# Kernel optimization log

Measured on AMD Instinct MI355X. Metric: run time of the kernel, lower is better.

Reference implementation:

```python
import jax, jax.numpy as jnp
import numpy as np

INS, OUTS = 768, 64
B, S = 8, 2048


def setup_inputs() -> dict:
    key = jax.random.key(0)
    ks = jax.random.split(key, 7)
    scale = 1.0 / np.sqrt(INS)
    inputs = jax.random.normal(ks[0], (B, S, INS), dtype=jnp.float32)
    Wq = jax.random.uniform(ks[1], (INS, OUTS), jnp.float32, -scale, scale)
    bq = jax.random.uniform(ks[2], (OUTS,), jnp.float32, -scale, scale)
    Wk = jax.random.uniform(ks[3], (INS, OUTS), jnp.float32, -scale, scale)
    bk = jax.random.uniform(ks[4], (OUTS,), jnp.float32, -scale, scale)
    Wv = jax.random.uniform(ks[5], (INS, OUTS), jnp.float32, -scale, scale)
    bv = jax.random.uniform(ks[6], (OUTS,), jnp.float32, -scale, scale)
    return {"inputs": inputs, "Wq": Wq, "bq": bq, "Wk": Wk, "bk": bk, "Wv": Wv, "bv": bv}


def reference(inputs, Wq, bq, Wk, bk, Wv, bv):
    # QKV projections: [B, S, ins] @ [ins, outs] -> [B, S, outs]
    q = jnp.einsum('bsi,io->bso', inputs, Wq) + bq
    k = jnp.einsum('bsi,io->bso', inputs, Wk) + bk
    v = jnp.einsum('bsi,io->bso', inputs, Wv) + bv
    dim_k = k.shape[-1]
    # scores: [B, S, S] (materialized, as in the original bmm-based impl)
    att = jnp.einsum('bqd,bkd->bqk', q, k) / jnp.sqrt(jnp.asarray(dim_k, q.dtype))
    att_soft = jax.nn.softmax(att, axis=-1)
    out = jnp.einsum('bqk,bkd->bqd', att_soft, v)
    return out
```

## Files before the change

kernel.cpp:

```cpp
#include <hip/hip_runtime.h>
#include <hip/hip_bf16.h>
#include <stdint.h>

#define INS 768
#define OUTS 64
#define BB 8
#define SS 2048
#define LDP 40

typedef __attribute__((ext_vector_type(8))) short short8;
typedef __attribute__((ext_vector_type(4))) float f32x4;

__device__ inline unsigned short f2bf(float f) {
  union { float f; uint32_t u; } v; v.f = f;
  uint32_t r = v.u + 0x7FFFu + ((v.u >> 16) & 1u);
  return (unsigned short)(r >> 16);
}

__device__ inline short8 cvt8hw(float4 a, float4 b) {
  union { __hip_bfloat162 h[4]; short8 s; } u;
  u.h[0] = __float22bfloat162_rn(make_float2(a.x, a.y));
  u.h[1] = __float22bfloat162_rn(make_float2(a.z, a.w));
  u.h[2] = __float22bfloat162_rn(make_float2(b.x, b.y));
  u.h[3] = __float22bfloat162_rn(make_float2(b.z, b.w));
  return u.s;
}

__device__ inline void gl_lds16(const void* g, void* l) {
  __builtin_amdgcn_global_load_lds(
      (const __attribute__((address_space(1))) uint32_t*)g,
      (__attribute__((address_space(3))) uint32_t*)l, 16, 0, 0);
}

__device__ inline void memfence_sched() { asm volatile("" ::: "memory"); }

#define PIPE_BARRIER(N)                                        \
  do {                                                         \
    asm volatile("s_waitcnt vmcnt(" #N ")" ::: "memory");      \
    __builtin_amdgcn_s_barrier();                              \
    __builtin_amdgcn_sched_barrier(0);                         \
  } while (0)

__global__ __launch_bounds__(256) void prep(
    const float* __restrict__ Wq, const float* __restrict__ Wk,
    const float* __restrict__ Wv, unsigned short* __restrict__ WT) {
  const int idx = blockIdx.x * 256 + threadIdx.x;
  const int m = idx / (INS * OUTS);
  const int r = idx - m * (INS * OUTS);
  const int k = r >> 6, n = r & 63;
  const float* W = (m == 0) ? Wq : (m == 1) ? Wk : Wv;
  const float s = (m == 0) ? 0.125f : 1.0f;
  WT[((size_t)m * OUTS + n) * INS + k] = f2bf(W[(size_t)k * OUTS + n] * s);
}

__global__ __launch_bounds__(256) void qkv(
    const float* __restrict__ X, const unsigned short* __restrict__ WT,
    const float* __restrict__ bq, const float* __restrict__ bk,
    const float* __restrict__ bv,
    unsigned short* __restrict__ Qg, unsigned short* __restrict__ Kg,
    unsigned short* __restrict__ Vtg) {
  __shared__ __align__(16) float Xs[4][1024];
  const int tid  = threadIdx.x;
  const int wave = tid >> 6, lane = tid & 63;
  const int quad = lane >> 4, l16 = lane & 15;
  const int chg  = wave;
  const int row0 = blockIdx.x * 32;

  const int sr = tid >> 3, ss = tid & 7;
  const char* gsrc =
      (const char*)(X + (size_t)(row0 + sr) * INS) + ((ss ^ (sr & 7)) << 4);
  char* ldsb = (char*)&Xs[0][0] + wave * 1024;

  const float* Bm[3]; float scl[3]; int col0[3];
  const unsigned short* Wt[3];
#pragma unroll
  for (int nt = 0; nt < 3; ++nt) {
    const int n0 = chg * 48 + nt * 16;
    const int mat = n0 >> 6;
    col0[nt] = n0 & 63;
    Wt[nt] = WT + ((size_t)mat * OUTS + col0[nt] + l16) * INS + quad * 8;
    if (mat == 0)      { Bm[nt] = bq; scl[nt] = 0.125f; }
    else if (mat == 1) { Bm[nt] = bk; scl[nt] = 1.0f; }
    else               { Bm[nt] = bv; scl[nt] = 1.0f; }
  }

  int off0[2], off1[2];
#pragma unroll
  for (int fr = 0; fr < 2; ++fr) {
    const int lr = fr * 16 + l16;
    off0[fr] = lr * 128 + ((((quad << 1)    ) ^ (lr & 7)) << 4);
    off1[fr] = lr * 128 + ((((quad << 1) | 1) ^ (lr & 7)) << 4);
  }

  f32x4 acc[2][3];
#pragma unroll
  for (int fr = 0; fr < 2; ++fr)
#pragma unroll
    for (int nt = 0; nt < 3; ++nt) acc[fr][nt] = (f32x4){0.f, 0.f, 0.f, 0.f};

  short8 wb[3][3];

  gl_lds16(gsrc, ldsb);
#pragma unroll
  for (int nt = 0; nt < 3; ++nt)
    wb[0][nt] = *reinterpret_cast<const short8*>(Wt[nt]);
  memfence_sched();
  gl_lds16(gsrc + 128, ldsb + 4096);
  gl_lds16(gsrc + 256, ldsb + 8192);
#pragma unroll
  for (int nt = 0; nt < 3; ++nt)
    wb[1][nt] = *reinterpret_cast<const short8*>(Wt[nt] + 32);

#pragma unroll
  for (int kc = 0; kc < 24; ++kc) {
    if (kc <= 21)      PIPE_BARRIER(4);
    else if (kc == 22) PIPE_BARRIER(3);
    else               PIPE_BARRIER(0);

    const char* xb = (const char*)&Xs[0][0] + (kc & 3) * 4096;
    float4 f00 = *reinterpret_cast<const float4*>(xb + off0[0]);
    float4 f01 = *reinterpret_cast<const float4*>(xb + off1[0]);
    float4 f10 = *reinterpret_cast<const float4*>(xb + off0[1]);
    float4 f11 = *reinterpret_cast<const float4*>(xb + off1[1]);
    short8 a0 = cvt8hw(f00, f01);
    short8 a1 = cvt8hw(f10, f11);
#pragma unroll
    for (int nt = 0; nt < 3; ++nt) {
      acc[0][nt] = __builtin_amdgcn_mfma_f32_16x16x32_bf16(a0, wb[kc % 3][nt], acc[0][nt], 0, 0, 0);
      acc[1][nt] = __builtin_amdgcn_mfma_f32_16x16x32_bf16(a1, wb[kc % 3][nt], acc[1][nt], 0, 0, 0);
    }
    if (kc + 3 < 24)
      gl_lds16(gsrc + (size_t)(kc + 3) * 128, ldsb + (size_t)((kc + 3) & 3) * 4096);
    if (kc + 2 < 24) {
#pragma unroll
      for (int nt = 0; nt < 3; ++nt)
        wb[(kc + 2) % 3][nt] =
            *reinterpret_cast<const short8*>(Wt[nt] + (kc + 2) * 32);
    }
  }

#pragma unroll
  for (int fr = 0; fr < 2; ++fr) {
    const int gm0 = row0 + fr * 16 + quad * 4;
#pragma unroll
    for (int nt = 0; nt < 3; ++nt) {
      const int n = chg * 48 + nt * 16 + l16;
      const float bias = Bm[nt][col0[nt] + l16] * scl[nt];
      if (n < 128) {
        unsigned short* dstbase = (n < 64) ? Qg : Kg;
        const int nn = n & 63;
#pragma unroll
        for (int r = 0; r < 4; ++r)
          dstbase[(size_t)(gm0 + r) * OUTS + nn] = f2bf(acc[fr][nt][r] + bias);
      } else {
        const int d = n - 128;
        const int batch = gm0 >> 11, s0 = gm0 & 2047;
        ushort4 pk;
        pk.x = f2bf(acc[fr][nt][0] + bias);
        pk.y = f2bf(acc[fr][nt][1] + bias);
        pk.z = f2bf(acc[fr][nt][2] + bias);
        pk.w = f2bf(acc[fr][nt][3] + bias);
        *reinterpret_cast<ushort4*>(&Vtg[((size_t)batch * OUTS + d) * SS + s0]) = pk;
      }
    }
  }
}

__global__ __launch_bounds__(256) void attn(
    const unsigned short* __restrict__ Qg, const unsigned short* __restrict__ Kg,
    const unsigned short* __restrict__ Vtg,
    float* __restrict__ OP, float* __restrict__ LS) {
  __shared__ __align__(16) char KsB[3][4096];
  __shared__ __align__(16) char VsB[3][4096];
  __shared__ __align__(16) unsigned short Ps[4][2][16 * LDP];
  const int tid  = threadIdx.x;
  const int wave = tid >> 6, lane = tid & 63;
  const int quad = lane >> 4, l16 = lane & 15;
  const int bt  = blockIdx.x >> 6;
  const int rem = blockIdx.x & 63;
  const int qb  = rem >> 2, ksl = rem & 3;
  const int q0 = qb * 128 + wave * 32;
  const unsigned short* Qb = Qg + (size_t)bt * SS * OUTS;
  const unsigned short* Kb = Kg + (size_t)bt * SS * OUTS;
  const unsigned short* Vb = Vtg + (size_t)bt * OUTS * SS;
  const int jbeg = ksl * 512;

  const int krow = wave * 8 + (lane >> 3), ks8 = lane & 7;
  const int vrow = wave * 16 + (lane >> 2), vs4 = lane & 3;
  const int vsw  = (vrow & 3) ^ ((vrow >> 2) & 3);
  const char* ksrc = (const char*)(Kb + (size_t)(jbeg + krow) * OUTS) +
                     ((ks8 ^ (krow & 7)) << 4);
  const char* vsrc = (const char*)(Vb + (size_t)vrow * SS + jbeg) +
                     ((vs4 ^ vsw) << 4);

#define STAGE(kc)                                                            \
  do {                                                                       \
    gl_lds16(ksrc + (size_t)(kc) * 4096, &KsB[(kc) % 3][0] + wave * 1024);   \
    gl_lds16(vsrc + (size_t)(kc) * 64,   &VsB[(kc) % 3][0] + wave * 1024);   \
  } while (0)

  short8 aq[2][2];
#pragma unroll
  for (int mh = 0; mh < 2; ++mh)
#pragma unroll
    for (int ks = 0; ks < 2; ++ks)
      aq[mh][ks] = *reinterpret_cast<const short8*>(
          Qb + (size_t)(q0 + mh * 16 + l16) * OUTS + ks * 32 + quad * 8);

  int koff[2][2];
#pragma unroll
  for (int nt2 = 0; nt2 < 2; ++nt2)
#pragma unroll
    for (int ks = 0; ks < 2; ++ks)
      koff[nt2][ks] = (nt2 * 16 + l16) * 128 +
                      ((((ks << 2) | quad) ^ (l16 & 7)) << 4);
  int voff[4];
#pragma unroll
  for (int nt = 0; nt < 4; ++nt) {
    const int dr = nt * 16 + l16;
    voff[nt] = dr * 64 + ((quad ^ ((dr & 3) ^ ((dr >> 2) & 3))) << 4);
  }

  f32x4 oacc[2][4];
#pragma unroll
  for (int mh = 0; mh < 2; ++mh)
#pragma unroll
    for (int nt = 0; nt < 4; ++nt) oacc[mh][nt] = (f32x4){0.f, 0.f, 0.f, 0.f};
  float lsum[2][4] = {{0.f,0.f,0.f,0.f},{0.f,0.f,0.f,0.f}};

  memfence_sched();
  STAGE(0);
  STAGE(1);

#pragma unroll
  for (int kc = 0; kc < 16; ++kc) {
    if (kc <= 14) PIPE_BARRIER(2);
    else          PIPE_BARRIER(0);

    const char* kb8 = &KsB[kc % 3][0];
    const char* vb8 = &VsB[kc % 3][0];
    short8 bk[2][2], bv[4];
#pragma unroll
    for (int nt2 = 0; nt2 < 2; ++nt2)
#pragma unroll
      for (int ks = 0; ks < 2; ++ks)
        bk[nt2][ks] = *reinterpret_cast<const short8*>(kb8 + koff[nt2][ks]);
#pragma unroll
    for (int nt = 0; nt < 4; ++nt)
      bv[nt] = *reinterpret_cast<const short8*>(vb8 + voff[nt]);

#pragma unroll
    for (int mh = 0; mh < 2; ++mh) {
      f32x4 sc[2];
      sc[0] = (f32x4){0.f,0.f,0.f,0.f}; sc[1] = (f32x4){0.f,0.f,0.f,0.f};
#pragma unroll
      for (int ks = 0; ks < 2; ++ks)
#pragma unroll
        for (int nt2 = 0; nt2 < 2; ++nt2)
          sc[nt2] = __builtin_amdgcn_mfma_f32_16x16x32_bf16(aq[mh][ks], bk[nt2][ks], sc[nt2], 0, 0, 0);

      unsigned short* Pw = &Ps[wave][mh][0];
#pragma unroll
      for (int nt2 = 0; nt2 < 2; ++nt2)
#pragma unroll
        for (int r = 0; r < 4; ++r) {
          float p = __expf(sc[nt2][r]);
          lsum[mh][r] += p;
          Pw[(quad * 4 + r) * LDP + nt2 * 16 + l16] = f2bf(p);
        }
      short8 ap = *reinterpret_cast<const short8*>(&Pw[l16 * LDP + quad * 8]);
#pragma unroll
      for (int nt = 0; nt < 4; ++nt)
        oacc[mh][nt] = __builtin_amdgcn_mfma_f32_16x16x32_bf16(ap, bv[nt], oacc[mh][nt], 0, 0, 0);
    }

    if (kc + 2 < 16) STAGE(kc + 2);
  }
#undef STAGE

#pragma unroll
  for (int st = 1; st < 16; st <<= 1)
#pragma unroll
    for (int mh = 0; mh < 2; ++mh)
#pragma unroll
      for (int r = 0; r < 4; ++r) lsum[mh][r] += __shfl_xor(lsum[mh][r], st, 64);

  float* OPb = OP + ((size_t)ksl * BB + bt) * SS * OUTS;
#pragma unroll
  for (int mh = 0; mh < 2; ++mh)
#pragma unroll
    for (int nt = 0; nt < 4; ++nt)
#pragma unroll
      for (int r = 0; r < 4; ++r) {
        int q = q0 + mh * 16 + quad * 4 + r;
        OPb[(size_t)q * OUTS + nt * 16 + l16] = oacc[mh][nt][r];
      }
  if (l16 == 0) {
#pragma unroll
    for (int mh = 0; mh < 2; ++mh)
#pragma unroll
      for (int r = 0; r < 4; ++r)
        LS[(size_t)ksl * BB * SS + bt * SS + q0 + mh * 16 + quad * 4 + r] = lsum[mh][r];
  }
}

__global__ __launch_bounds__(256) void combine(
    const float* __restrict__ OP, const float* __restrict__ LS,
    float* __restrict__ out) {
  const size_t i4 = (size_t)blockIdx.x * 256 + threadIdx.x;
  const size_t row = (i4 * 4) >> 6;
  float4 o = make_float4(0.f, 0.f, 0.f, 0.f);
  float l = 0.f;
#pragma unroll
  for (int ks = 0; ks < 4; ++ks) {
    float4 t = reinterpret_cast<const float4*>(OP + (size_t)ks * BB * SS * OUTS)[i4];
    o.x += t.x; o.y += t.y; o.z += t.z; o.w += t.w;
    l += LS[(size_t)ks * BB * SS + row];
  }
  const float inv = 1.0f / l;
  reinterpret_cast<float4*>(out)[i4] = make_float4(o.x * inv, o.y * inv, o.z * inv, o.w * inv);
}

extern "C" void kernel_launch(void* const* d_in, const int* in_sizes, int n_in,
                              void* d_out, int out_size, void* d_ws, size_t ws_size,
                              hipStream_t stream) {
  const float* X  = (const float*)d_in[0];
  const float* Wq = (const float*)d_in[1];
  const float* bq = (const float*)d_in[2];
  const float* Wk = (const float*)d_in[3];
  const float* bk = (const float*)d_in[4];
  const float* Wv = (const float*)d_in[5];
  const float* bv = (const float*)d_in[6];
  float* out = (float*)d_out;

  char* ws = (char*)d_ws;
  unsigned short* Qg  = (unsigned short*)(ws);
  unsigned short* Kg  = (unsigned short*)(ws + (size_t)2 * 1024 * 1024);
  unsigned short* Vtg = (unsigned short*)(ws + (size_t)4 * 1024 * 1024);
  unsigned short* WT  = (unsigned short*)(ws + (size_t)6 * 1024 * 1024);
  float*          OP  = (float*)(ws + (size_t)7 * 1024 * 1024);
  float*          LS  = (float*)(ws + (size_t)23 * 1024 * 1024);

  prep<<<576, 256, 0, stream>>>(Wq, Wk, Wv, WT);
  qkv<<<512, 256, 0, stream>>>(X, WT, bq, bk, bv, Qg, Kg, Vtg);
  attn<<<512, 256, 0, stream>>>(Qg, Kg, Vtg, OP, LS);
  combine<<<1024, 256, 0, stream>>>(OP, LS, out);
}
```

Baseline: 138.6 us.

## Split QKV projection K dimension across two wave groups with LDS reduction

The qkv kernel now launches 512 threads per block, and two groups of four waves each handle half of the 768-wide reduction dimension, each with its own LDS staging buffers. At the end, the second group writes its partial accumulators to shared memory and the first group adds them before applying bias and storing. This halves the serial K-loop length per wave and doubles the waves per block to hide memory latency better. The cost is extra LDS use, two block barriers and a reduction step, with possibly lower block occupancy.

```diff
diff --git a/kernel.cpp b/kernel.cpp
--- a/kernel.cpp
+++ b/kernel.cpp
@@ -53,23 +53,25 @@
   WT[((size_t)m * OUTS + n) * INS + k] = f2bf(W[(size_t)k * OUTS + n] * s);
 }
 
-__global__ __launch_bounds__(256) void qkv(
+__global__ __launch_bounds__(512) void qkv(
     const float* __restrict__ X, const unsigned short* __restrict__ WT,
     const float* __restrict__ bq, const float* __restrict__ bk,
     const float* __restrict__ bv,
     unsigned short* __restrict__ Qg, unsigned short* __restrict__ Kg,
     unsigned short* __restrict__ Vtg) {
-  __shared__ __align__(16) float Xs[4][1024];
+  __shared__ __align__(16) float Xs[2][4][1024];
+  __shared__ float Cbuf[4][64][25];
   const int tid  = threadIdx.x;
   const int wave = tid >> 6, lane = tid & 63;
+  const int chg  = wave & 3, kh = wave >> 2;
   const int quad = lane >> 4, l16 = lane & 15;
-  const int chg  = wave;
   const int row0 = blockIdx.x * 32;
 
-  const int sr = tid >> 3, ss = tid & 7;
+  const int sr = chg * 8 + (lane >> 3), ss = lane & 7;
   const char* gsrc =
-      (const char*)(X + (size_t)(row0 + sr) * INS) + ((ss ^ (sr & 7)) << 4);
-  char* ldsb = (char*)&Xs[0][0] + wave * 1024;
+      (const char*)(X + (size_t)(row0 + sr) * INS + kh * 384) +
+      ((ss ^ (sr & 7)) << 4);
+  char* ldsb = (char*)&Xs[kh][0][0] + chg * 1024;
 
   const float* Bm[3]; float scl[3]; int col0[3];
   const unsigned short* Wt[3];
@@ -78,7 +80,7 @@
     const int n0 = chg * 48 + nt * 16;
     const int mat = n0 >> 6;
     col0[nt] = n0 & 63;
-    Wt[nt] = WT + ((size_t)mat * OUTS + col0[nt] + l16) * INS + quad * 8;
+    Wt[nt] = WT + ((size_t)mat * OUTS + col0[nt] + l16) * INS + kh * 384 + quad * 8;
     if (mat == 0)      { Bm[nt] = bq; scl[nt] = 0.125f; }
     else if (mat == 1) { Bm[nt] = bk; scl[nt] = 1.0f; }
     else               { Bm[nt] = bv; scl[nt] = 1.0f; }
@@ -112,12 +114,12 @@
     wb[1][nt] = *reinterpret_cast<const short8*>(Wt[nt] + 32);
 
 #pragma unroll
-  for (int kc = 0; kc < 24; ++kc) {
-    if (kc <= 21)      PIPE_BARRIER(4);
-    else if (kc == 22) PIPE_BARRIER(3);
+  for (int kc = 0; kc < 12; ++kc) {
+    if (kc <= 9)       PIPE_BARRIER(4);
+    else if (kc == 10) PIPE_BARRIER(3);
     else               PIPE_BARRIER(0);
 
-    const char* xb = (const char*)&Xs[0][0] + (kc & 3) * 4096;
+    const char* xb = (const char*)&Xs[kh][0][0] + (kc & 3) * 4096;
     float4 f00 = *reinterpret_cast<const float4*>(xb + off0[0]);
     float4 f01 = *reinterpret_cast<const float4*>(xb + off1[0]);
     float4 f10 = *reinterpret_cast<const float4*>(xb + off0[1]);
@@ -129,9 +131,9 @@
       acc[0][nt] = __builtin_amdgcn_mfma_f32_16x16x32_bf16(a0, wb[kc % 3][nt], acc[0][nt], 0, 0, 0);
       acc[1][nt] = __builtin_amdgcn_mfma_f32_16x16x32_bf16(a1, wb[kc % 3][nt], acc[1][nt], 0, 0, 0);
     }
-    if (kc + 3 < 24)
+    if (kc + 3 < 12)
       gl_lds16(gsrc + (size_t)(kc + 3) * 128, ldsb + (size_t)((kc + 3) & 3) * 4096);
-    if (kc + 2 < 24) {
+    if (kc + 2 < 12) {
 #pragma unroll
       for (int nt = 0; nt < 3; ++nt)
         wb[(kc + 2) % 3][nt] =
@@ -139,28 +141,49 @@
     }
   }
 
-#pragma unroll
-  for (int fr = 0; fr < 2; ++fr) {
-    const int gm0 = row0 + fr * 16 + quad * 4;
-#pragma unroll
-    for (int nt = 0; nt < 3; ++nt) {
-      const int n = chg * 48 + nt * 16 + l16;
-      const float bias = Bm[nt][col0[nt] + l16] * scl[nt];
-      if (n < 128) {
-        unsigned short* dstbase = (n < 64) ? Qg : Kg;
-        const int nn = n & 63;
+  __syncthreads();
+  if (kh == 1) {
+#pragma unroll
+    for (int fr = 0; fr < 2; ++fr)
+#pragma unroll
+      for (int nt = 0; nt < 3; ++nt)
 #pragma unroll
         for (int r = 0; r < 4; ++r)
-          dstbase[(size_t)(gm0 + r) * OUTS + nn] = f2bf(acc[fr][nt][r] + bias);
-      } else {
-        const int d = n - 128;
-        const int batch = gm0 >> 11, s0 = gm0 & 2047;
-        ushort4 pk;
-        pk.x = f2bf(acc[fr][nt][0] + bias);
-        pk.y = f2bf(acc[fr][nt][1] + bias);
-        pk.z = f2bf(acc[fr][nt][2] + bias);
-        pk.w = f2bf(acc[fr][nt][3] + bias);
-        *reinterpret_cast<ushort4*>(&Vtg[((size_t)batch * OUTS + d) * SS + s0]) = pk;
+          Cbuf[chg][lane][fr * 12 + nt * 4 + r] = acc[fr][nt][r];
+  }
+  __syncthreads();
+  if (kh == 0) {
+#pragma unroll
+    for (int fr = 0; fr < 2; ++fr)
+#pragma unroll
+      for (int nt = 0; nt < 3; ++nt)
+#pragma unroll
+        for (int r = 0; r < 4; ++r)
+          acc[fr][nt][r] += Cbuf[chg][lane][fr * 12 + nt * 4 + r];
+
+#pragma unroll
+    for (int fr = 0; fr < 2; ++fr) {
+      const int gm0 = row0 + fr * 16 + quad * 4;
+#pragma unroll
+      for (int nt = 0; nt < 3; ++nt) {
+        const int n = chg * 48 + nt * 16 + l16;
+        const float bias = Bm[nt][col0[nt] + l16] * scl[nt];
+        if (n < 128) {
+          unsigned short* dstbase = (n < 64) ? Qg : Kg;
+          const int nn = n & 63;
+#pragma unroll
+          for (int r = 0; r < 4; ++r)
+            dstbase[(size_t)(gm0 + r) * OUTS + nn] = f2bf(acc[fr][nt][r] + bias);
+        } else {
+          const int d = n - 128;
+          const int batch = gm0 >> 11, s0 = gm0 & 2047;
+          ushort4 pk;
+          pk.x = f2bf(acc[fr][nt][0] + bias);
+          pk.y = f2bf(acc[fr][nt][1] + bias);
+          pk.z = f2bf(acc[fr][nt][2] + bias);
+          pk.w = f2bf(acc[fr][nt][3] + bias);
+          *reinterpret_cast<ushort4*>(&Vtg[((size_t)batch * OUTS + d) * SS + s0]) = pk;
+        }
       }
     }
   }
@@ -342,7 +365,7 @@
   float*          LS  = (float*)(ws + (size_t)23 * 1024 * 1024);
 
   prep<<<576, 256, 0, stream>>>(Wq, Wk, Wv, WT);
-  qkv<<<512, 256, 0, stream>>>(X, WT, bq, bk, bv, Qg, Kg, Vtg);
+  qkv<<<512, 512, 0, stream>>>(X, WT, bq, bk, bv, Qg, Kg, Vtg);
   attn<<<512, 256, 0, stream>>>(Qg, Kg, Vtg, OP, LS);
   combine<<<1024, 256, 0, stream>>>(OP, LS, out);
 }
```

Measured after the change: 139.7 us. Within noise of the previous version (+0.8%).

## Fuse split-K combine into attention via last-block atomic counter

Applied to the files above, without the earlier changes.

Removes the separate combine kernel. Each attention block increments a per-(batch, query-block) counter after writing its partial output and row sums, and the fourth block to arrive reduces the four partials and writes the normalized output. The counters are zeroed in the prep kernel. This saves one kernel launch and its scheduling gap, at the cost of a threadfence plus atomic in every block and a serialized tail reduction in the last-arriving blocks.

```diff
diff --git a/kernel.cpp b/kernel.cpp
--- a/kernel.cpp
+++ b/kernel.cpp
@@ -43,7 +43,9 @@
 
 __global__ __launch_bounds__(256) void prep(
     const float* __restrict__ Wq, const float* __restrict__ Wk,
-    const float* __restrict__ Wv, unsigned short* __restrict__ WT) {
+    const float* __restrict__ Wv, unsigned short* __restrict__ WT,
+    int* __restrict__ Cnt) {
+  if (blockIdx.x == 0 && threadIdx.x < 128) Cnt[threadIdx.x] = 0;
   const int idx = blockIdx.x * 256 + threadIdx.x;
   const int m = idx / (INS * OUTS);
   const int r = idx - m * (INS * OUTS);
@@ -169,10 +171,12 @@
 __global__ __launch_bounds__(256) void attn(
     const unsigned short* __restrict__ Qg, const unsigned short* __restrict__ Kg,
     const unsigned short* __restrict__ Vtg,
-    float* __restrict__ OP, float* __restrict__ LS) {
+    float* __restrict__ OP, float* __restrict__ LS,
+    int* __restrict__ Cnt, float* __restrict__ out) {
   __shared__ __align__(16) char KsB[3][4096];
   __shared__ __align__(16) char VsB[3][4096];
   __shared__ __align__(16) unsigned short Ps[4][2][16 * LDP];
+  __shared__ int lastFlag;
   const int tid  = threadIdx.x;
   const int wave = tid >> 6, lane = tid & 63;
   const int quad = lane >> 4, l16 = lane & 15;
@@ -302,23 +306,35 @@
       for (int r = 0; r < 4; ++r)
         LS[(size_t)ksl * BB * SS + bt * SS + q0 + mh * 16 + quad * 4 + r] = lsum[mh][r];
   }
-}
-
-__global__ __launch_bounds__(256) void combine(
-    const float* __restrict__ OP, const float* __restrict__ LS,
-    float* __restrict__ out) {
-  const size_t i4 = (size_t)blockIdx.x * 256 + threadIdx.x;
-  const size_t row = (i4 * 4) >> 6;
-  float4 o = make_float4(0.f, 0.f, 0.f, 0.f);
-  float l = 0.f;
-#pragma unroll
-  for (int ks = 0; ks < 4; ++ks) {
-    float4 t = reinterpret_cast<const float4*>(OP + (size_t)ks * BB * SS * OUTS)[i4];
-    o.x += t.x; o.y += t.y; o.z += t.z; o.w += t.w;
-    l += LS[(size_t)ks * BB * SS + row];
-  }
-  const float inv = 1.0f / l;
-  reinterpret_cast<float4*>(out)[i4] = make_float4(o.x * inv, o.y * inv, o.z * inv, o.w * inv);
+
+  __threadfence();
+  __syncthreads();
+  if (tid == 0) {
+    int old = atomicAdd(&Cnt[bt * 16 + qb], 1);
+    lastFlag = (old == 3);
+  }
+  __syncthreads();
+  if (!lastFlag) return;
+  __threadfence();
+
+#pragma unroll
+  for (int i = 0; i < 8; ++i) {
+    const int t = tid + i * 256;
+    const int q  = qb * 128 + (t >> 4);
+    const int c4 = t & 15;
+    float4 o = make_float4(0.f, 0.f, 0.f, 0.f);
+    float l = 0.f;
+#pragma unroll
+    for (int ks = 0; ks < 4; ++ks) {
+      const size_t i4g = (((size_t)ks * BB + bt) * SS + q) * 16 + c4;
+      float4 v = reinterpret_cast<const float4*>(OP)[i4g];
+      o.x += v.x; o.y += v.y; o.z += v.z; o.w += v.w;
+      l += LS[(size_t)ks * BB * SS + bt * SS + q];
+    }
+    const float inv = 1.0f / l;
+    reinterpret_cast<float4*>(out)[((size_t)bt * SS + q) * 16 + c4] =
+        make_float4(o.x * inv, o.y * inv, o.z * inv, o.w * inv);
+  }
 }
 
 extern "C" void kernel_launch(void* const* d_in, const int* in_sizes, int n_in,
@@ -340,9 +356,9 @@
   unsigned short* WT  = (unsigned short*)(ws + (size_t)6 * 1024 * 1024);
   float*          OP  = (float*)(ws + (size_t)7 * 1024 * 1024);
   float*          LS  = (float*)(ws + (size_t)23 * 1024 * 1024);
-
-  prep<<<576, 256, 0, stream>>>(Wq, Wk, Wv, WT);
+  int*            Cnt = (int*)(ws + (size_t)24 * 1024 * 1024);
+
+  prep<<<576, 256, 0, stream>>>(Wq, Wk, Wv, WT, Cnt);
   qkv<<<512, 256, 0, stream>>>(X, WT, bq, bk, bv, Qg, Kg, Vtg);
-  attn<<<512, 256, 0, stream>>>(Qg, Kg, Vtg, OP, LS);
-  combine<<<1024, 256, 0, stream>>>(OP, LS, out);
-}
+  attn<<<512, 256, 0, stream>>>(Qg, Kg, Vtg, OP, LS, Cnt, out);
+}
```

Result: slower. 221.5 us (+59.8%).
